# Kernel optimization log

Hardware: AMD Instinct MI355X
Metric: run time of the kernel (lower is better)

Reference implementation:

```python
import jax, jax.numpy as jnp
import numpy as np

BN_EPS = 1e-5
NUM_SUBSET = 3


def conv1x1(x, w, b):
    # x: [N, C, T, V], w: [O, C], b: [O]  (1x1 Conv2d)
    return jnp.einsum('nctv,oc->notv', x, w) + b[:, None, None]


def setup_inputs() -> dict:
    key = jax.random.key(0)
    ks = jax.random.split(key, 8)
    N, C, T, V = 64, 64, 300, 25
    IC = 16  # inter_c = out_channels // coff_embedding
    O = 64
    inp = {
        'x': jax.random.normal(ks[0], (N, C, T, V), dtype=jnp.float32),
        'A': jax.random.uniform(ks[1], (NUM_SUBSET, V, V), dtype=jnp.float32),
        'graph_attn': jnp.ones((NUM_SUBSET, V, V), dtype=jnp.float32),
        'g_w': jax.random.normal(ks[2], (NUM_SUBSET, O, C), dtype=jnp.float32) * 0.05,
        'g_b': jnp.zeros((NUM_SUBSET, O), dtype=jnp.float32),
        'a_w': jax.random.normal(ks[3], (NUM_SUBSET, IC, C), dtype=jnp.float32) * 0.05,
        'a_b': jnp.zeros((NUM_SUBSET, IC), dtype=jnp.float32),
        'b_w': jax.random.normal(ks[4], (NUM_SUBSET, IC, C), dtype=jnp.float32) * 0.05,
        'b_b': jnp.zeros((NUM_SUBSET, IC), dtype=jnp.float32),
        'bn_gamma': jnp.ones((O,), dtype=jnp.float32),
        'bn_beta': jnp.zeros((O,), dtype=jnp.float32),
        'bn_mean': jnp.zeros((O,), dtype=jnp.float32),
        'bn_var': jnp.ones((O,), dtype=jnp.float32),
    }
    return inp


def reference(x, A, graph_attn, g_w, g_b, a_w, a_b, b_w, b_b,
              bn_gamma, bn_beta, bn_mean, bn_var):
    N, C, T, V = x.shape
    IC = a_w.shape[1]
    A_tot = A + graph_attn  # [3, V, V]
    x_flat = x.reshape(N, C * T, V)
    hidden = None
    for i in range(NUM_SUBSET):
        # a_conv -> permute(0,3,1,2) -> [N, V, IC*T]
        A1 = conv1x1(x, a_w[i], a_b[i]).transpose(0, 3, 1, 2).reshape(N, V, IC * T)
        # b_conv -> [N, IC*T, V]
        A2 = conv1x1(x, b_w[i], b_b[i]).reshape(N, IC * T, V)
        attn = jax.nn.softmax(jnp.matmul(A1, A2) / (IC * T), axis=-2)  # [N, V, V], softmax over rows
        attn = attn + A_tot[i]
        z = jnp.matmul(x_flat, attn).reshape(N, C, T, V)
        z = conv1x1(z, g_w[i], g_b[i])
        hidden = z if hidden is None else hidden + z
    # BatchNorm2d in eval mode over channel dim
    inv = jax.lax.rsqrt(bn_var + BN_EPS)
    hidden = (hidden - bn_mean[:, None, None]) * (inv * bn_gamma)[:, None, None] + bn_beta[:, None, None]
    # in_channels == out_channels -> identity residual
    hidden = hidden + x
    return jax.nn.relu(hidden)
```

## Files before the change

### kernel.cpp

```cpp
#include <hip/hip_runtime.h>
#include <hip/hip_bf16.h>


#define NB 64
#define CB 64
#define TB 300
#define VB 25

typedef unsigned int uint32;
typedef unsigned short ushort16;
typedef __attribute__((ext_vector_type(8))) short short8;
typedef __attribute__((ext_vector_type(4))) float f32x4;
typedef __attribute__((ext_vector_type(16))) float f32x16;

__device__ __forceinline__ ushort16 f2bf(float f) {
    __hip_bfloat16 h = __float2bfloat16(f);
    ushort16 u;
    __builtin_memcpy(&u, &h, sizeof(u));
    return u;
}
__device__ __forceinline__ float bf2f(ushort16 h) {
    return __uint_as_float(((uint32)h) << 16);
}
__device__ __forceinline__ uint32 packbf2(float a, float b) {
    return (uint32)f2bf(a) | ((uint32)f2bf(b) << 16);
}

__global__ __launch_bounds__(256) void k0_prep(
    const float* __restrict__ a_w, const float* __restrict__ b_w,
    const float* __restrict__ g_w,
    ushort16* __restrict__ wb2, uint32* __restrict__ gwb)
{
    int idx = blockIdx.x * 256 + threadIdx.x;
    if (idx < 6144) {
        int kb = idx / 768, rem = idx % 768;
        int r = rem >> 3, ci = rem & 7;
        int c = kb * 8 + ci;
        float v = (r < 48) ? a_w[r * 64 + c] : b_w[(r - 48) * 64 + c];
        wb2[idx] = f2bf(v);
    } else if (idx < 12288) {
        int j = idx - 6144;
        int o = j / 96, kp = j % 96;
        int k0 = 2 * kp, i = k0 >> 6, c = k0 & 63;
        float2 lh = *(const float2*)(g_w + (i * 64 + o) * 64 + c);
        gwb[j] = packbf2(lh.x, lh.y);
    }
}

__global__ __launch_bounds__(256) void k1_attn_logits_mfma(
    const float* __restrict__ x, const ushort16* __restrict__ wb2,
    const float* __restrict__ a_b, const float* __restrict__ b_b,
    float* __restrict__ Mb)
{
    __shared__ ushort16 pool[20352];
    ushort16* xT  = pool;
    ushort16* abT = pool + 126 * 64;

    const int tid   = threadIdx.x;
    const int n     = blockIdx.x / 25;
    const int chunk = blockIdx.x % 25;
    const float* xn = x + n * (CB * TB * VB);

    if (tid < 96) {
        float v = (tid < 48) ? a_b[tid] : b_b[tid - 48];
        ((float*)(abT + (31 + (tid >> 5) * 32) * 64))[tid & 31] = v;
    }

    const int w    = tid >> 6;
    const int lane = tid & 63;
    const int hi   = lane >> 5;
    const int v32  = lane & 31;

    const float* xb0 = xn + chunk * 12 * 25;

    const int tv     = w * 32 + v32;
    const bool avalid = tv < 100;
    const int tl = tv / 25;
    const int vv = tv - tl * 25;

    f32x16 accB;
    #pragma unroll
    for (int r = 0; r < 16; ++r) accB[r] = 0.f;

    for (int s = 0; s < 3; ++s) {
        __syncthreads();
        const float* xs0 = xb0 + s * 100;
        #pragma unroll
        for (int k = 0; k < 7; ++k) {
            int idx = tid + k * 256;
            if (idx < 1600) {
                int c = idx / 25, j = idx - c * 25;
                float4 v4 = *(const float4*)(xs0 + c * 7500 + j * 4);
                int sb   = ((c >> 3) + 5 * j) & 7;
                int base = (4 * j) * 64 + (c & 7);
                xT[base +   0 + (((sb + 0) & 7) << 3)] = f2bf(v4.x);
                xT[base +  64 + (((sb + 1) & 7) << 3)] = f2bf(v4.y);
                xT[base + 128 + (((sb + 2) & 7) << 3)] = f2bf(v4.z);
                xT[base + 192 + (((sb + 3) & 7) << 3)] = f2bf(v4.w);
            }
        }
        __syncthreads();
        #pragma unroll
        for (int rt = 0; rt < 3; ++rt) {
            f32x16 d;
            #pragma unroll
            for (int r = 0; r < 16; ++r) d[r] = 0.f;
            #pragma unroll
            for (int k16 = 0; k16 < 4; ++k16) {
                int kb = k16 * 2 + hi;
                short8 af = *(const short8*)(wb2 + (kb * 96 + rt * 32 + v32) * 8);
                short8 bf = *(const short8*)&xT[tv * 64 +
                                                (((kb + tv + (tv >> 2)) & 7) << 3)];
                d = __builtin_amdgcn_mfma_f32_32x32x16_bf16(af, bf, d, 0, 0, 0);
            }
            if (avalid) {
                #pragma unroll
                for (int a = 0; a < 4; ++a) {
                    int rowoff = 8 * a + 4 * hi;
                    int g   = rt * 2 + (rowoff >> 4);
                    int icb = rowoff & 15;
                    float4 bq = *(const float4*)(
                        (const float*)(abT + (31 + rt * 32) * 64) + rowoff);
                    int kbw = tl * 2 + (icb >> 3);
                    uint32* dst = (uint32*)&abT[(g * 32 + vv) * 64 +
                                                (((kbw + vv) & 7) << 3) + (icb & 7)];
                    dst[0] = packbf2(d[4 * a + 0] + bq.x, d[4 * a + 1] + bq.y);
                    dst[1] = packbf2(d[4 * a + 2] + bq.z, d[4 * a + 3] + bq.w);
                }
            }
        }
        __syncthreads();
        if (w < 3) {
            #pragma unroll
            for (int tl2 = 0; tl2 < 4; ++tl2) {
                int kb = tl2 * 2 + hi;
                short8 af = *(const short8*)&abT[(w * 32 + v32) * 64 +
                                                 (((kb + v32) & 7) << 3)];
                short8 bf = *(const short8*)&abT[((3 + w) * 32 + v32) * 64 +
                                                 (((kb + v32) & 7) << 3)];
                accB = __builtin_amdgcn_mfma_f32_32x32x16_bf16(af, bf, accB, 0, 0, 0);
            }
        }
    }

    if (w < 3 && v32 < 25) {
        const float inv = 1.0f / 4800.0f;
        #pragma unroll
        for (int r = 0; r < 16; ++r) {
            int row = (r & 3) + 8 * (r >> 2) + 4 * hi;
            if (row < 25)
                atomicAdd(Mb + ((w * NB + n) * 25 + row) * 25 + v32, accB[r] * inv);
        }
    }
}

__global__ __launch_bounds__(128) void k2_softmax(
    const float* __restrict__ Mb, const float* __restrict__ A,
    const float* __restrict__ GA, uint32* __restrict__ atT)
{
    __shared__ float Ms[640];
    const int b   = blockIdx.x;
    const int tid = threadIdx.x;
    const int i = b >> 6, n = b & 63;
    const float* src = Mb + b * 625;
    for (int idx = tid; idx < 625; idx += 128) Ms[idx] = src[idx];
    __syncthreads();
    if (tid < 25) {
        const int v2 = tid;
        float e[25], mx = -1e30f;
        #pragma unroll
        for (int v1 = 0; v1 < 25; ++v1) {
            e[v1] = Ms[v1 * 25 + v2];
            mx = fmaxf(mx, e[v1]);
        }
        float s = 0.f;
        #pragma unroll
        for (int v1 = 0; v1 < 25; ++v1) { e[v1] = __expf(e[v1] - mx); s += e[v1]; }
        float invs = 1.0f / s;
        const float* acol = A + i * 625 + v2;
        const float* gcol = GA + i * 625 + v2;
        float wv[25];
        #pragma unroll
        for (int v1 = 0; v1 < 25; ++v1)
            wv[v1] = e[v1] * invs + acol[v1 * 25] + gcol[v1 * 25];
        uint32* row = atT + ((i * 64 + n) * 32 + v2) * 16;
        #pragma unroll
        for (int p = 0; p < 12; ++p) row[p] = packbf2(wv[2 * p], wv[2 * p + 1]);
        row[12] = (uint32)f2bf(wv[24]);
        row[13] = 0u; row[14] = 0u; row[15] = 0u;
    }
}

__global__ __launch_bounds__(256) void k3_out(
    const float* __restrict__ x, const uint32* __restrict__ atT,
    const ushort16* __restrict__ gwb, const float* __restrict__ g_b,
    const float* __restrict__ bn_g, const float* __restrict__ bn_b,
    const float* __restrict__ bn_m, const float* __restrict__ bn_v,
    float* __restrict__ out)
{
    __shared__ ushort16 xs[64 * 168];
    __shared__ uint32  xa[128 * 36];
    __shared__ uint32  ats[3 * 32 * 20];
    __shared__ float   bsc[64], bsh[64];

    const int tid = threadIdx.x;
    const int n  = blockIdx.x / 60;
    const int t0 = (blockIdx.x % 60) * 5;

    for (int idx = tid; idx < 8000; idx += 256) {
        int c = idx / 125, tv = idx % 125;
        int t = tv / 25, v = tv % 25;
        float g = x[((n * 64 + c) * 300 + t0 + t) * 25 + v];
        xs[c * 168 + t * 32 + v] = f2bf(g);
    }
    for (int idx = tid; idx < 64 * 35; idx += 256) {
        int c = idx / 35, r = idx % 35;
        xs[c * 168 + (r / 7) * 32 + 25 + (r % 7)] = (ushort16)0;
    }
    for (int idx = tid; idx < 1536; idx += 256) {
        int row = idx >> 4, d = idx & 15;
        ats[row * 20 + d] = atT[((row >> 5) * 64 + n) * 512 + (row & 31) * 16 + d];
    }
    for (int idx = tid; idx < 64; idx += 256) {
        float sc = bn_g[idx] * rsqrtf(bn_v[idx] + 1e-5f);
        bsc[idx] = sc;
        bsh[idx] = (g_b[idx] + g_b[64 + idx] + g_b[128 + idx] - bn_m[idx]) * sc + bn_b[idx];
    }
    for (int idx = tid; idx < 3 * 36; idx += 256)
        xa[(125 + idx / 36) * 36 + idx % 36] = 0u;

    const int w    = tid >> 6;
    const int lane = tid & 63;
    const int l15  = lane & 15;
    const int q    = lane >> 4;

    short8 gf[6];
    #pragma unroll
    for (int s = 0; s < 6; ++s)
        gf[s] = *(const short8*)(gwb + ((w * 16 + l15) * 192 + s * 32 + q * 8));

    f32x4 acc[8];
    #pragma unroll
    for (int ct = 0; ct < 8; ++ct) acc[ct] = (f32x4){0.f, 0.f, 0.f, 0.f};
    const f32x4 zf = (f32x4){0.f, 0.f, 0.f, 0.f};

    __syncthreads();

    for (int i = 0; i < 3; ++i) {
        if (i) __syncthreads();
        #pragma unroll
        for (int t = 0; t < 5; ++t) {
            short8 ax = *(const short8*)(xs + (w * 16 + l15) * 168 + t * 32 + q * 8);
            #pragma unroll
            for (int vt = 0; vt < 2; ++vt) {
                short8 bt = *(const short8*)((const ushort16*)ats +
                                             (i * 32 + vt * 16 + l15) * 40 + q * 8);
                f32x4 d = __builtin_amdgcn_mfma_f32_16x16x32_bf16(ax, bt, zf, 0, 0, 0);
                int v2 = vt * 16 + l15;
                if (v2 < 25) {
                    int col = t * 25 + v2;
                    int c0  = w * 16 + q * 4;
                    xa[col * 36 + (c0 >> 1)]     = packbf2(d[0], d[1]);
                    xa[col * 36 + (c0 >> 1) + 1] = packbf2(d[2], d[3]);
                }
            }
        }
        __syncthreads();
        #pragma unroll
        for (int ct = 0; ct < 8; ++ct) {
            #pragma unroll
            for (int s = 0; s < 2; ++s) {
                short8 bfrag = *(const short8*)((const ushort16*)xa +
                                                (ct * 16 + l15) * 72 + s * 32 + q * 8);
                acc[ct] = __builtin_amdgcn_mfma_f32_16x16x32_bf16(
                    gf[i * 2 + s], bfrag, acc[ct], 0, 0, 0);
            }
        }
    }

    const int o0 = w * 16 + q * 4;
    #pragma unroll
    for (int ct = 0; ct < 8; ++ct) {
        int col = ct * 16 + l15;
        if (col < 125) {
            int tl = col / 25;
            int v  = col - tl * 25;
            float* ob = out + (n * 64 + o0) * 7500 + t0 * 25 + col;
            #pragma unroll
            for (int r = 0; r < 4; ++r) {
                int o = o0 + r;
                float xv = bf2f(xs[o * 168 + tl * 32 + v]);
                float h = acc[ct][r] * bsc[o] + bsh[o] + xv;
                ob[r * 7500] = fmaxf(h, 0.f);
            }
        }
    }
}

extern "C" void kernel_launch(void* const* d_in, const int* in_sizes, int n_in,
                              void* d_out, int out_size, void* d_ws, size_t ws_size,
                              hipStream_t stream) {
    const float* x    = (const float*)d_in[0];
    const float* A    = (const float*)d_in[1];
    const float* GA   = (const float*)d_in[2];
    const float* g_w  = (const float*)d_in[3];
    const float* g_b  = (const float*)d_in[4];
    const float* a_w  = (const float*)d_in[5];
    const float* a_b  = (const float*)d_in[6];
    const float* b_w  = (const float*)d_in[7];
    const float* b_b  = (const float*)d_in[8];
    const float* bn_g = (const float*)d_in[9];
    const float* bn_b = (const float*)d_in[10];
    const float* bn_m = (const float*)d_in[11];
    const float* bn_v = (const float*)d_in[12];
    float* out = (float*)d_out;

    float*    Mb  = (float*)d_ws;
    uint32*   atT = (uint32*)((char*)d_ws + 480000);
    ushort16* wb2 = (ushort16*)((char*)d_ws + 480000);
    uint32*   gwb = (uint32*)((char*)d_ws + 480000 + 393216);

    hipMemsetAsync(d_ws, 0, 480000, stream);
    k0_prep<<<dim3(48), dim3(256), 0, stream>>>(a_w, b_w, g_w, wb2, gwb);
    k1_attn_logits_mfma<<<dim3(1600), dim3(256), 0, stream>>>(x, wb2, a_b, b_b, Mb);
    k2_softmax<<<dim3(192), dim3(128), 0, stream>>>(Mb, A, GA, atT);
    k3_out<<<dim3(3840), dim3(256), 0, stream>>>(x, atT, (const ushort16*)gwb,
                                                 g_b, bn_g, bn_b, bn_m, bn_v, out);
}
```

Baseline: 356.3 us.

## Load x fragments and attention directly into registers in output kernel; fold memset

The output kernel no longer stages x and the attention matrices in shared memory. Each lane builds its bf16 MFMA A-fragment straight from global x, reads the attention B-fragments straight from global memory, and takes the residual from fp32 global x. This cuts LDS use and the staging loads and barriers, which should allow more resident blocks, at the cost of unaligned scalar global loads. The A-fragments also pick up data past the 25 valid joints, which only contributes zero because the padded attention entries are zero. Separately, the workspace memset is folded into the prep kernel, removing one launch.

Result: faster. 343.3 us (-3.6%).

```diff
diff --git a/kernel.cpp b/kernel.cpp
--- a/kernel.cpp
+++ b/kernel.cpp
@@ -6,6 +6,7 @@
 #define CB 64
 #define TB 300
 #define VB 25
+#define XTOT (NB * CB * TB * VB)
 
 typedef unsigned int uint32;
 typedef unsigned short ushort16;
@@ -29,9 +30,11 @@
 __global__ __launch_bounds__(256) void k0_prep(
     const float* __restrict__ a_w, const float* __restrict__ b_w,
     const float* __restrict__ g_w,
-    ushort16* __restrict__ wb2, uint32* __restrict__ gwb)
+    ushort16* __restrict__ wb2, uint32* __restrict__ gwb,
+    float* __restrict__ Mb)
 {
     int idx = blockIdx.x * 256 + threadIdx.x;
+    for (int z = idx; z < 120000; z += 12288) Mb[z] = 0.f;
     if (idx < 6144) {
         int kb = idx / 768, rem = idx % 768;
         int r = rem >> 3, ci = rem & 7;
@@ -198,35 +201,20 @@
     const float* __restrict__ bn_m, const float* __restrict__ bn_v,
     float* __restrict__ out)
 {
-    __shared__ ushort16 xs[64 * 168];
-    __shared__ uint32  xa[128 * 36];
-    __shared__ uint32  ats[3 * 32 * 20];
-    __shared__ float   bsc[64], bsh[64];
+    __shared__ uint32 xa[128 * 36];
+    __shared__ float  bsc[64], bsh[64];
 
     const int tid = threadIdx.x;
     const int n  = blockIdx.x / 60;
     const int t0 = (blockIdx.x % 60) * 5;
 
-    for (int idx = tid; idx < 8000; idx += 256) {
-        int c = idx / 125, tv = idx % 125;
-        int t = tv / 25, v = tv % 25;
-        float g = x[((n * 64 + c) * 300 + t0 + t) * 25 + v];
-        xs[c * 168 + t * 32 + v] = f2bf(g);
-    }
-    for (int idx = tid; idx < 64 * 35; idx += 256) {
-        int c = idx / 35, r = idx % 35;
-        xs[c * 168 + (r / 7) * 32 + 25 + (r % 7)] = (ushort16)0;
-    }
-    for (int idx = tid; idx < 1536; idx += 256) {
-        int row = idx >> 4, d = idx & 15;
-        ats[row * 20 + d] = atT[((row >> 5) * 64 + n) * 512 + (row & 31) * 16 + d];
-    }
-    for (int idx = tid; idx < 64; idx += 256) {
-        float sc = bn_g[idx] * rsqrtf(bn_v[idx] + 1e-5f);
-        bsc[idx] = sc;
-        bsh[idx] = (g_b[idx] + g_b[64 + idx] + g_b[128 + idx] - bn_m[idx]) * sc + bn_b[idx];
-    }
-    for (int idx = tid; idx < 3 * 36; idx += 256)
+    if (tid < 64) {
+        float sc = bn_g[tid] * rsqrtf(bn_v[tid] + 1e-5f);
+        bsc[tid] = sc;
+        bsh[tid] = (g_b[tid] + g_b[64 + tid] + g_b[128 + tid] - bn_m[tid]) * sc
+                   + bn_b[tid];
+    }
+    for (int idx = tid; idx < 108; idx += 256)
         xa[(125 + idx / 36) * 36 + idx % 36] = 0u;
 
     const int w    = tid >> 6;
@@ -239,6 +227,22 @@
     for (int s = 0; s < 6; ++s)
         gf[s] = *(const short8*)(gwb + ((w * 16 + l15) * 192 + s * 32 + q * 8));
 
+    const int c    = w * 16 + l15;
+    const int rowf = (n * 64 + c) * 7500 + t0 * 25;
+    short8 axf[5];
+    #pragma unroll
+    for (int t = 0; t < 5; ++t) {
+        int fi = rowf + t * 25 + q * 8;
+        fi = fi < (XTOT - 8) ? fi : (XTOT - 8);
+        const float* p = x + fi;
+        union { short8 s; uint32 u[4]; } fr;
+        fr.u[0] = packbf2(p[0], p[1]);
+        fr.u[1] = packbf2(p[2], p[3]);
+        fr.u[2] = packbf2(p[4], p[5]);
+        fr.u[3] = packbf2(p[6], p[7]);
+        axf[t] = fr.s;
+    }
+
     f32x4 acc[8];
     #pragma unroll
     for (int ct = 0; ct < 8; ++ct) acc[ct] = (f32x4){0.f, 0.f, 0.f, 0.f};
@@ -248,14 +252,15 @@
 
     for (int i = 0; i < 3; ++i) {
         if (i) __syncthreads();
+        const ushort16* ap = (const ushort16*)atT + ((i * 64 + n) * 32) * 32;
+        short8 bt0 = *(const short8*)(ap + l15 * 32 + q * 8);
+        short8 bt1 = *(const short8*)(ap + (16 + l15) * 32 + q * 8);
         #pragma unroll
         for (int t = 0; t < 5; ++t) {
-            short8 ax = *(const short8*)(xs + (w * 16 + l15) * 168 + t * 32 + q * 8);
             #pragma unroll
             for (int vt = 0; vt < 2; ++vt) {
-                short8 bt = *(const short8*)((const ushort16*)ats +
-                                             (i * 32 + vt * 16 + l15) * 40 + q * 8);
-                f32x4 d = __builtin_amdgcn_mfma_f32_16x16x32_bf16(ax, bt, zf, 0, 0, 0);
+                f32x4 d = __builtin_amdgcn_mfma_f32_16x16x32_bf16(
+                    axf[t], vt ? bt1 : bt0, zf, 0, 0, 0);
                 int v2 = vt * 16 + l15;
                 if (v2 < 25) {
                     int col = t * 25 + v2;
@@ -283,14 +288,12 @@
     for (int ct = 0; ct < 8; ++ct) {
         int col = ct * 16 + l15;
         if (col < 125) {
-            int tl = col / 25;
-            int v  = col - tl * 25;
-            float* ob = out + (n * 64 + o0) * 7500 + t0 * 25 + col;
+            int off = (n * 64 + o0) * 7500 + t0 * 25 + col;
+            float* ob = out + off;
+            const float* xb = x + off;
             #pragma unroll
             for (int r = 0; r < 4; ++r) {
-                int o = o0 + r;
-                float xv = bf2f(xs[o * 168 + tl * 32 + v]);
-                float h = acc[ct][r] * bsc[o] + bsh[o] + xv;
+                float h = acc[ct][r] * bsc[o0 + r] + bsh[o0 + r] + xb[r * 7500];
                 ob[r * 7500] = fmaxf(h, 0.f);
             }
         }
@@ -320,8 +323,7 @@
     ushort16* wb2 = (ushort16*)((char*)d_ws + 480000);
     uint32*   gwb = (uint32*)((char*)d_ws + 480000 + 393216);
 
-    hipMemsetAsync(d_ws, 0, 480000, stream);
-    k0_prep<<<dim3(48), dim3(256), 0, stream>>>(a_w, b_w, g_w, wb2, gwb);
+    k0_prep<<<dim3(48), dim3(256), 0, stream>>>(a_w, b_w, g_w, wb2, gwb, Mb);
     k1_attn_logits_mfma<<<dim3(1600), dim3(256), 0, stream>>>(x, wb2, a_b, b_b, Mb);
     k2_softmax<<<dim3(192), dim3(128), 0, stream>>>(Mb, A, GA, atT);
     k3_out<<<dim3(3840), dim3(256), 0, stream>>>(x, atT, (const ushort16*)gwb,
```
